# Performance work log

Measured on AMD Instinct MI355X. Metric: run time of the kernel, lower is better.

Reference implementation:

```python
import jax, jax.numpy as jnp
import numpy as np

S, N, B, E = 16, 256, 32, 256
NUM_NODE_TYPES = 128
NUM_VAL_TOKENS = 50000
NNZ = 524288
ROWS = S * N * B  # 131072


def setup_inputs() -> dict:
    key = jax.random.key(0)
    k1, k2, k3, k4, k5, k6 = jax.random.split(key, 6)
    node_idx = jax.random.randint(k1, (S, N, B), 0, NUM_NODE_TYPES, dtype=jnp.int64)
    spmm_rows = jnp.sort(jax.random.randint(k2, (NNZ,), 0, ROWS, dtype=jnp.int64))
    spmm_cols = jax.random.randint(k3, (NNZ,), 0, NUM_VAL_TOKENS, dtype=jnp.int64)
    spmm_vals = jax.random.uniform(k4, (NNZ,), dtype=jnp.float32)
    node_embed_w = jax.random.normal(k5, (NUM_NODE_TYPES, E), dtype=jnp.float32)
    # _param_init ~ small uniform init; exact distribution irrelevant for correctness baseline
    val_tok_embed = jax.random.normal(k6, (NUM_VAL_TOKENS, E), dtype=jnp.float32) * 0.05
    return {
        "node_idx": node_idx,
        "spmm_rows": spmm_rows,
        "spmm_cols": spmm_cols,
        "spmm_vals": spmm_vals,
        "node_embed_w": node_embed_w,
        "val_tok_embed": val_tok_embed,
    }


def reference(node_idx, spmm_rows, spmm_cols, spmm_vals, node_embed_w, val_tok_embed):
    # Dense embedding gather: (S, N, B) -> (S, N, B, E)
    node_embed = node_embed_w[node_idx]
    s, n, b, e = node_embed.shape
    # Sparse (ROWS x NUM_VAL_TOKENS) @ (NUM_VAL_TOKENS x E) as gather + segment_sum
    gathered = val_tok_embed[spmm_cols] * spmm_vals[:, None]  # (NNZ, E)
    node_val_embed = jax.ops.segment_sum(
        gathered, spmm_rows, num_segments=s * n * b, indices_are_sorted=True
    ).reshape(s, n, b, e)
    return node_embed, node_val_embed
```

## Files before the change

kernel.cpp:

```cpp
#include <hip/hip_runtime.h>

#define ROWS_ 131072
#define NNZ_  524288
#define E4_   64
#define LOG2NNZ_ 19
#define CONV_BLOCKS_ 6250
#define RP_BLOCKS_   513
#define OUT1_BLOCKS_ 32768
#define TOKB_OFF_ (1u << 20)

typedef float f32x4 __attribute__((ext_vector_type(4)));
typedef unsigned int u32x2 __attribute__((ext_vector_type(2)));
typedef unsigned int u32x4 __attribute__((ext_vector_type(4)));

__global__ __launch_bounds__(256) void k1_kernel(
    const int*   __restrict__ rows,
    int*         __restrict__ row_start,
    const u32x4* __restrict__ tok_f32,
    u32x4*       __restrict__ tok_bf16,
    const int*   __restrict__ node_idx,
    const f32x4* __restrict__ w,
    f32x4*       __restrict__ out1) {

    int bid = blockIdx.x;
    if (bid < CONV_BLOCKS_) {
        int t = bid * 256 + threadIdx.x;
        u32x4 a = __builtin_nontemporal_load(&tok_f32[2 * t]);
        u32x4 b = __builtin_nontemporal_load(&tok_f32[2 * t + 1]);
        u32x4 o;
        #pragma unroll
        for (int k = 0; k < 2; ++k) {
            u32x4 s = k ? b : a;
            unsigned r0 = (s[0] + 0x7FFFu + ((s[0] >> 16) & 1u)) >> 16;
            unsigned r1 = (s[1] + 0x7FFFu + ((s[1] >> 16) & 1u)) >> 16;
            unsigned r2 = (s[2] + 0x7FFFu + ((s[2] >> 16) & 1u)) >> 16;
            unsigned r3 = (s[3] + 0x7FFFu + ((s[3] >> 16) & 1u)) >> 16;
            o[2 * k]     = r0 | (r1 << 16);
            o[2 * k + 1] = r2 | (r3 << 16);
        }
        tok_bf16[t] = o;
    } else if (bid < CONV_BLOCKS_ + RP_BLOCKS_) {
        int r = (bid - CONV_BLOCKS_) * 256 + threadIdx.x;
        if (r > ROWS_) return;
        int lo = 0, hi = NNZ_;
        #pragma unroll
        for (int it = 0; it < LOG2NNZ_; ++it) {
            int mid = (lo + hi) >> 1;
            if (rows[mid] < r) lo = mid + 1; else hi = mid;
        }
        row_start[r] = lo;
    } else {
        int tid  = (bid - CONV_BLOCKS_ - RP_BLOCKS_) * 256 + threadIdx.x;
        int row  = tid >> 6;
        int l    = tid & 63;
        int node = node_idx[row];
        f32x4 t0 = w[node * E4_ + l];
        __builtin_nontemporal_store(t0, &out1[tid]);
    }
}

__global__ __launch_bounds__(256) void spmm_kernel(
    const int*   __restrict__ row_start,
    const int*   __restrict__ cols,
    const float* __restrict__ vals,
    const u32x2* __restrict__ tokb,
    f32x4*       __restrict__ out2) {

    int gtid = blockIdx.x * blockDim.x + threadIdx.x;
    int row  = gtid >> 6;
    int lane = threadIdx.x & 63;

    int start = row_start[row];
    int end   = row_start[row + 1];
    int cnt   = end - start;

    f32x4 acc = (f32x4)(0.f);
    for (int base = 0; base < cnt; base += 64) {
        int rem = cnt - base;
        int nn  = rem > 64 ? 64 : rem;
        int idx = start + base + lane;
        bool valid = lane < nn;
        int   c_l = valid ? cols[idx] : 0;
        float v_l = valid ? vals[idx] : 0.f;

        for (int j = 0; j < nn; j += 4) {
            int   ca = __builtin_amdgcn_readlane(c_l, j);
            int   cb = __builtin_amdgcn_readlane(c_l, j + 1);
            int   cc = __builtin_amdgcn_readlane(c_l, j + 2);
            int   cd = __builtin_amdgcn_readlane(c_l, j + 3);
            float va = __int_as_float(__builtin_amdgcn_readlane(__float_as_int(v_l), j));
            float vb = __int_as_float(__builtin_amdgcn_readlane(__float_as_int(v_l), j + 1));
            float vc = __int_as_float(__builtin_amdgcn_readlane(__float_as_int(v_l), j + 2));
            float vd = __int_as_float(__builtin_amdgcn_readlane(__float_as_int(v_l), j + 3));

            u32x2 ga = tokb[(size_t)ca * E4_ + lane];
            u32x2 gb = tokb[(size_t)cb * E4_ + lane];
            u32x2 gc = tokb[(size_t)cc * E4_ + lane];
            u32x2 gd = tokb[(size_t)cd * E4_ + lane];

            f32x4 ta, tb, tc, td;
            ta[0] = __int_as_float(ga[0] << 16); ta[1] = __int_as_float(ga[0] & 0xFFFF0000u);
            ta[2] = __int_as_float(ga[1] << 16); ta[3] = __int_as_float(ga[1] & 0xFFFF0000u);
            tb[0] = __int_as_float(gb[0] << 16); tb[1] = __int_as_float(gb[0] & 0xFFFF0000u);
            tb[2] = __int_as_float(gb[1] << 16); tb[3] = __int_as_float(gb[1] & 0xFFFF0000u);
            tc[0] = __int_as_float(gc[0] << 16); tc[1] = __int_as_float(gc[0] & 0xFFFF0000u);
            tc[2] = __int_as_float(gc[1] << 16); tc[3] = __int_as_float(gc[1] & 0xFFFF0000u);
            td[0] = __int_as_float(gd[0] << 16); td[1] = __int_as_float(gd[0] & 0xFFFF0000u);
            td[2] = __int_as_float(gd[1] << 16); td[3] = __int_as_float(gd[1] & 0xFFFF0000u);

            acc += va * ta;
            acc += vb * tb;
            acc += vc * tc;
            acc += vd * td;
        }
    }
    __builtin_nontemporal_store(acc, &out2[(size_t)row * E4_ + lane]);
}

extern "C" void kernel_launch(void* const* d_in, const int* in_sizes, int n_in,
                              void* d_out, int out_size, void* d_ws, size_t ws_size,
                              hipStream_t stream) {
    const int*   node_idx  = (const int*)d_in[0];
    const int*   spmm_rows = (const int*)d_in[1];
    const int*   spmm_cols = (const int*)d_in[2];
    const float* spmm_vals = (const float*)d_in[3];
    const float* node_w    = (const float*)d_in[4];
    const float* tok       = (const float*)d_in[5];

    f32x4* out1 = (f32x4*)d_out;
    f32x4* out2 = out1 + (size_t)ROWS_ * E4_;
    int*   row_start = (int*)d_ws;
    u32x4* tok_bf16  = (u32x4*)((char*)d_ws + TOKB_OFF_);

    k1_kernel<<<CONV_BLOCKS_ + RP_BLOCKS_ + OUT1_BLOCKS_, 256, 0, stream>>>(
        spmm_rows, row_start, (const u32x4*)tok, tok_bf16,
        node_idx, (const f32x4*)node_w, out1);

    spmm_kernel<<<ROWS_ / 4, 256, 0, stream>>>(
        row_start, spmm_cols, spmm_vals, (const u32x2*)tok_bf16, out2);
}
```

Measured before the change: 93.46 us.

## Split SpMM into two column-half passes to shrink gather working set

The SpMM is split into two launches, each handling one half of the embedding columns (128 bf16 values, 256 bytes per token row). Each pass gathers 4-byte words instead of 8-byte words, so the bf16 table slice touched per pass is half as large and more likely to stay cached. The cost is reading row_start, cols and vals twice, doing the index broadcasts twice, paying a second launch, and issuing narrower loads and stores.

```diff
diff --git a/kernel.cpp b/kernel.cpp
--- a/kernel.cpp
+++ b/kernel.cpp
@@ -9,8 +9,8 @@
 #define OUT1_BLOCKS_ 32768
 #define TOKB_OFF_ (1u << 20)
 
+typedef float f32x2 __attribute__((ext_vector_type(2)));
 typedef float f32x4 __attribute__((ext_vector_type(4)));
-typedef unsigned int u32x2 __attribute__((ext_vector_type(2)));
 typedef unsigned int u32x4 __attribute__((ext_vector_type(4)));
 
 __global__ __launch_bounds__(256) void k1_kernel(
@@ -59,12 +59,13 @@
     }
 }
 
-__global__ __launch_bounds__(256) void spmm_kernel(
-    const int*   __restrict__ row_start,
-    const int*   __restrict__ cols,
-    const float* __restrict__ vals,
-    const u32x2* __restrict__ tokb,
-    f32x4*       __restrict__ out2) {
+__global__ __launch_bounds__(256) void spmm_half_kernel(
+    const int*      __restrict__ row_start,
+    const int*      __restrict__ cols,
+    const float*    __restrict__ vals,
+    const unsigned* __restrict__ tokb,
+    f32x2*          __restrict__ out2,
+    int off) {
 
     int gtid = blockIdx.x * blockDim.x + threadIdx.x;
     int row  = gtid >> 6;
@@ -74,7 +75,7 @@
     int end   = row_start[row + 1];
     int cnt   = end - start;
 
-    f32x4 acc = (f32x4)(0.f);
+    f32x2 acc = (f32x2)(0.f);
     for (int base = 0; base < cnt; base += 64) {
         int rem = cnt - base;
         int nn  = rem > 64 ? 64 : rem;
@@ -93,20 +94,16 @@
             float vc = __int_as_float(__builtin_amdgcn_readlane(__float_as_int(v_l), j + 2));
             float vd = __int_as_float(__builtin_amdgcn_readlane(__float_as_int(v_l), j + 3));
 
-            u32x2 ga = tokb[(size_t)ca * E4_ + lane];
-            u32x2 gb = tokb[(size_t)cb * E4_ + lane];
-            u32x2 gc = tokb[(size_t)cc * E4_ + lane];
-            u32x2 gd = tokb[(size_t)cd * E4_ + lane];
+            unsigned ga = tokb[(size_t)ca * 128 + off + lane];
+            unsigned gb = tokb[(size_t)cb * 128 + off + lane];
+            unsigned gc = tokb[(size_t)cc * 128 + off + lane];
+            unsigned gd = tokb[(size_t)cd * 128 + off + lane];
 
-            f32x4 ta, tb, tc, td;
-            ta[0] = __int_as_float(ga[0] << 16); ta[1] = __int_as_float(ga[0] & 0xFFFF0000u);
-            ta[2] = __int_as_float(ga[1] << 16); ta[3] = __int_as_float(ga[1] & 0xFFFF0000u);
-            tb[0] = __int_as_float(gb[0] << 16); tb[1] = __int_as_float(gb[0] & 0xFFFF0000u);
-            tb[2] = __int_as_float(gb[1] << 16); tb[3] = __int_as_float(gb[1] & 0xFFFF0000u);
-            tc[0] = __int_as_float(gc[0] << 16); tc[1] = __int_as_float(gc[0] & 0xFFFF0000u);
-            tc[2] = __int_as_float(gc[1] << 16); tc[3] = __int_as_float(gc[1] & 0xFFFF0000u);
-            td[0] = __int_as_float(gd[0] << 16); td[1] = __int_as_float(gd[0] & 0xFFFF0000u);
-            td[2] = __int_as_float(gd[1] << 16); td[3] = __int_as_float(gd[1] & 0xFFFF0000u);
+            f32x2 ta, tb, tc, td;
+            ta[0] = __int_as_float(ga << 16); ta[1] = __int_as_float(ga & 0xFFFF0000u);
+            tb[0] = __int_as_float(gb << 16); tb[1] = __int_as_float(gb & 0xFFFF0000u);
+            tc[0] = __int_as_float(gc << 16); tc[1] = __int_as_float(gc & 0xFFFF0000u);
+            td[0] = __int_as_float(gd << 16); td[1] = __int_as_float(gd & 0xFFFF0000u);
 
             acc += va * ta;
             acc += vb * tb;
@@ -114,7 +111,7 @@
             acc += vd * td;
         }
     }
-    __builtin_nontemporal_store(acc, &out2[(size_t)row * E4_ + lane]);
+    __builtin_nontemporal_store(acc, &out2[(size_t)row * 128 + off + lane]);
 }
 
 extern "C" void kernel_launch(void* const* d_in, const int* in_sizes, int n_in,
@@ -128,7 +125,7 @@
     const float* tok       = (const float*)d_in[5];
 
     f32x4* out1 = (f32x4*)d_out;
-    f32x4* out2 = out1 + (size_t)ROWS_ * E4_;
+    f32x2* out2 = (f32x2*)((float*)d_out + (size_t)ROWS_ * 256);
     int*   row_start = (int*)d_ws;
     u32x4* tok_bf16  = (u32x4*)((char*)d_ws + TOKB_OFF_);
 
@@ -136,6 +133,8 @@
         spmm_rows, row_start, (const u32x4*)tok, tok_bf16,
         node_idx, (const f32x4*)node_w, out1);
 
-    spmm_kernel<<<ROWS_ / 4, 256, 0, stream>>>(
-        row_start, spmm_cols, spmm_vals, (const u32x2*)tok_bf16, out2);
+    spmm_half_kernel<<<ROWS_ / 4, 256, 0, stream>>>(
+        row_start, spmm_cols, spmm_vals, (const unsigned*)tok_bf16, out2, 0);
+    spmm_half_kernel<<<ROWS_ / 4, 256, 0, stream>>>(
+        row_start, spmm_cols, spmm_vals, (const unsigned*)tok_bf16, out2, 64);
 }
```

Measured after the change: 109.8 us. +17.5%, slower.
